# Kernel optimization log

Hardware: AMD Instinct MI355X
Metric: run time of the kernel (lower is better)

Reference implementation:

```python
import jax, jax.numpy as jnp
import numpy as np

B, L, D, H = 4, 1024, 256, 8
TEMP = float(np.sqrt(D))
EPS_SM = 1e-6
EPS_LN = 1e-5


def setup_inputs() -> dict:
    key = jax.random.key(0)
    ks = jax.random.split(key, 8)
    std = float(np.sqrt(2.0 / (D * 2)))
    return {
        "q": jax.random.normal(ks[0], (B, L, D), jnp.float32),
        "mask": jax.random.randint(ks[1], (B, L, L), 0, 2, jnp.int32),
        "k": jax.random.normal(ks[2], (B, L, D), jnp.float32),
        "v": jax.random.normal(ks[3], (B, L, D), jnp.float32),
        "w_qs": jax.random.normal(ks[4], (H * D, D), jnp.float32) * std,
        "w_ks": jax.random.normal(ks[5], (H * D, D), jnp.float32) * std,
        "w_vs": jax.random.normal(ks[6], (H * D, D), jnp.float32) * std,
        "fc_w": jax.random.normal(ks[7], (D, H * D), jnp.float32) * float(np.sqrt(2.0 / (D + H * D))),
        "fc_b": jnp.zeros((D,), jnp.float32),
        "ln_g": jnp.ones((D,), jnp.float32),
        "ln_b": jnp.zeros((D,), jnp.float32),
    }


def masked_softmax(x, m):
    # repo's layers.masked_softmax: clamp, mask-mul, stable exp, mask-mul, normalize
    x = jnp.clip(x, -15.0, 15.0) * m
    e = jnp.exp(x - jnp.max(x, axis=-1, keepdims=True)) * m
    return e / (jnp.sum(e, axis=-1, keepdims=True) + EPS_SM)


def reference(q, mask, k, v, w_qs, w_ks, w_vs, fc_w, fc_b, ln_g, ln_b):
    residual = q
    m = mask.astype(q.dtype)[:, None, :, :]          # [B,1,Lq,Lk]
    # projections to per-head full-dim: [B,L,H,D]
    qh = (q @ w_qs.T).reshape(B, L, H, D)
    kh = (k @ w_ks.T).reshape(B, L, H, D)
    vh = (v @ w_vs.T).reshape(B, L, H, D)
    scores = jnp.einsum("bqhd,bkhd->bhqk", qh, kh) / TEMP   # [B,H,Lq,Lk]
    attn = masked_softmax(scores, m)
    out = jnp.einsum("bhqk,bkhd->bqhd", attn, vh).reshape(B, L, H * D)
    out = out @ fc_w.T + fc_b                         # [B,L,D]
    out = out + residual
    mu = jnp.mean(out, axis=-1, keepdims=True)
    var = jnp.var(out, axis=-1, keepdims=True)
    out = (out - mu) / jnp.sqrt(var + EPS_LN) * ln_g + ln_b
    # match torch attn layout: [H*B, Lq, Lk] (head-major)
    attn_hb = jnp.transpose(attn, (1, 0, 2, 3)).reshape(H * B, L, L)
    return out, attn_hb
```

## Files before the change

### kernel.cpp

```cpp
#include <hip/hip_runtime.h>
#include <cstdint>
#include <math.h>

#define Bsz 4
#define Lsz 1024
#define Dsz 256
#define Hsz 8
#define HD  2048
#define NROWS (Bsz*Lsz)
#define INV_TEMP 0.0625f

#define TM 128
#define TN 128
#define TK 32

typedef __attribute__((ext_vector_type(8))) short bf16x8;
typedef __attribute__((ext_vector_type(4))) float f32x4;

__device__ inline unsigned short f2bf(float f) {
    union { float f; unsigned u; } x; x.f = f;
    unsigned r = x.u + 0x7fffu + ((x.u >> 16) & 1u);
    return (unsigned short)(r >> 16);
}

#define GBL(p) ((const __attribute__((address_space(1))) unsigned int*)(p))
#define LDS(p) ((__attribute__((address_space(3))) unsigned int*)(p))

template <typename OutT>
__global__ __launch_bounds__(256) void gemm_bt_mfma(
    const unsigned short* __restrict__ A, const unsigned short* __restrict__ Bm,
    OutT* __restrict__ C,
    int K, int lda, int ldb, int ldc,
    int inner,
    long long sA1, long long sA2, long long sB1, long long sB2,
    long long sC1, long long sC2, float alpha)
{
    const int z  = blockIdx.z;
    const int i1 = z / inner;
    const int i2 = z % inner;
    A  += (size_t)i1 * sA1 + (size_t)i2 * sA2;
    Bm += (size_t)i1 * sB1 + (size_t)i2 * sB2;
    C  += (size_t)i1 * sC1 + (size_t)i2 * sC2;

    __shared__ unsigned short As[TM * TK];
    __shared__ unsigned short Bs[TN * TK];

    const int t    = threadIdx.x;
    const int lane = t & 63;
    const int w    = t >> 6;
    const int wm   = w & 1;
    const int wn   = w >> 1;
    const int m0   = blockIdx.x * TM;
    const int n0   = blockIdx.y * TN;

    const int sr = t >> 2;
    const int sc = (t & 3) * 8;
    const unsigned short* gA0 = A  + (size_t)(m0 + sr) * lda + sc;
    const unsigned short* gA1 = A  + (size_t)(m0 + 64 + sr) * lda + sc;
    const unsigned short* gB0 = Bm + (size_t)(n0 + sr) * ldb + sc;
    const unsigned short* gB1 = Bm + (size_t)(n0 + 64 + sr) * ldb + sc;
    unsigned short* lA0 = As + t * 8;
    unsigned short* lA1 = As + 64 * TK + t * 8;
    unsigned short* lB0 = Bs + t * 8;
    unsigned short* lB1 = Bs + 64 * TK + t * 8;

    const int fr = lane & 15;
    const int fk = (lane >> 4) * 8;
    const unsigned short* pA = As + (size_t)(wm * 64 + fr) * TK + fk;
    const unsigned short* pB = Bs + (size_t)(wn * 64 + fr) * TK + fk;

    f32x4 acc[4][4];
#pragma unroll
    for (int i = 0; i < 4; ++i)
#pragma unroll
        for (int j = 0; j < 4; ++j) acc[i][j] = (f32x4){0.f, 0.f, 0.f, 0.f};

    for (int k0 = 0; k0 < K; k0 += TK) {
        __builtin_amdgcn_global_load_lds(GBL(gA0 + k0), LDS(lA0), 16, 0, 0);
        __builtin_amdgcn_global_load_lds(GBL(gA1 + k0), LDS(lA1), 16, 0, 0);
        __builtin_amdgcn_global_load_lds(GBL(gB0 + k0), LDS(lB0), 16, 0, 0);
        __builtin_amdgcn_global_load_lds(GBL(gB1 + k0), LDS(lB1), 16, 0, 0);
        __syncthreads();

        bf16x8 a[4], b[4];
#pragma unroll
        for (int i = 0; i < 4; ++i) a[i] = *(const bf16x8*)(pA + i * 16 * TK);
#pragma unroll
        for (int j = 0; j < 4; ++j) b[j] = *(const bf16x8*)(pB + j * 16 * TK);
#pragma unroll
        for (int i = 0; i < 4; ++i)
#pragma unroll
            for (int j = 0; j < 4; ++j)
                acc[i][j] = __builtin_amdgcn_mfma_f32_16x16x32_bf16(a[i], b[j], acc[i][j], 0, 0, 0);
        __syncthreads();
    }

    const int er = (lane >> 4) * 4;
    const int ec = lane & 15;
#pragma unroll
    for (int i = 0; i < 4; ++i) {
        const int mb = m0 + wm * 64 + i * 16 + er;
#pragma unroll
        for (int j = 0; j < 4; ++j) {
            const int n = n0 + wn * 64 + j * 16 + ec;
#pragma unroll
            for (int r = 0; r < 4; ++r) {
                float vv = acc[i][j][r] * alpha;
                if constexpr (sizeof(OutT) == 4)
                    C[(size_t)(mb + r) * ldc + n] = (OutT)vv;
                else
                    ((unsigned short*)C)[(size_t)(mb + r) * ldc + n] = f2bf(vv);
            }
        }
    }
}

__global__ __launch_bounds__(256) void cast_all(
    const float* __restrict__ q, const float* __restrict__ k, const float* __restrict__ v,
    const float* __restrict__ wq, const float* __restrict__ wk, const float* __restrict__ wv,
    const float* __restrict__ fw,
    unsigned short* __restrict__ qb, unsigned short* __restrict__ kb, unsigned short* __restrict__ vb,
    unsigned short* __restrict__ wqb, unsigned short* __restrict__ wkb, unsigned short* __restrict__ wvb,
    unsigned short* __restrict__ fwb)
{
    const int gid = blockIdx.x * 256 + threadIdx.x;
    const int NQ = 262144;
    const int NW = 131072;
    const float* src; unsigned short* dst; int off;
    if      (gid < NQ)            { src = q;  dst = qb;  off = gid; }
    else if (gid < 2 * NQ)        { src = k;  dst = kb;  off = gid - NQ; }
    else if (gid < 3 * NQ)        { src = v;  dst = vb;  off = gid - 2 * NQ; }
    else if (gid < 3 * NQ + NW)   { src = wq; dst = wqb; off = gid - 3 * NQ; }
    else if (gid < 3 * NQ + 2*NW) { src = wk; dst = wkb; off = gid - 3 * NQ - NW; }
    else if (gid < 3 * NQ + 3*NW) { src = wv; dst = wvb; off = gid - 3 * NQ - 2 * NW; }
    else                          { src = fw; dst = fwb; off = gid - 3 * NQ - 3 * NW; }
    float4 f = ((const float4*)src)[off];
    ushort4 o;
    o.x = f2bf(f.x); o.y = f2bf(f.y); o.z = f2bf(f.z); o.w = f2bf(f.w);
    ((ushort4*)dst)[off] = o;
}

__global__ __launch_bounds__(256) void softmax_kernel(float* __restrict__ attn,
                                                      unsigned short* __restrict__ attn_bf,
                                                      const int* __restrict__ mask)
{
    const int r  = blockIdx.x;
    const int q  = r & (Lsz - 1);
    const int hb = r >> 10;
    const int b  = hb & (Bsz - 1);
    float* row = attn + (size_t)r * Lsz;
    unsigned short* row_bf = attn_bf + (size_t)r * Lsz;
    const int* mrow = mask + ((size_t)(b * Lsz + q)) * Lsz;

    const int t = threadIdx.x;
    float x[4], mv[4];
    float lmax = -1e30f;
#pragma unroll
    for (int i = 0; i < 4; ++i) {
        const int idx = t + i * 256;
        float xv = row[idx];
        float m  = (float)mrow[idx];
        xv = fminf(fmaxf(xv, -15.f), 15.f) * m;
        x[i] = xv; mv[i] = m;
        lmax = fmaxf(lmax, xv);
    }
    __shared__ float red[4];
#pragma unroll
    for (int o = 32; o > 0; o >>= 1) lmax = fmaxf(lmax, __shfl_down(lmax, o, 64));
    const int lane = t & 63, w = t >> 6;
    if (lane == 0) red[w] = lmax;
    __syncthreads();
    const float rmax = fmaxf(fmaxf(red[0], red[1]), fmaxf(red[2], red[3]));
    __syncthreads();

    float lsum = 0.f;
#pragma unroll
    for (int i = 0; i < 4; ++i) {
        float e = expf(x[i] - rmax) * mv[i];
        x[i] = e;
        lsum += e;
    }
#pragma unroll
    for (int o = 32; o > 0; o >>= 1) lsum += __shfl_down(lsum, o, 64);
    if (lane == 0) red[w] = lsum;
    __syncthreads();
    const float rsum = red[0] + red[1] + red[2] + red[3];
    const float inv = 1.0f / (rsum + 1e-6f);
#pragma unroll
    for (int i = 0; i < 4; ++i) {
        const float p = x[i] * inv;
        row[t + i * 256] = p;
        row_bf[t + i * 256] = f2bf(p);
    }
}

__global__ __launch_bounds__(256) void ln_kernel(const float* __restrict__ gout,
                                                 const float* __restrict__ qin,
                                                 const float* __restrict__ fc_b,
                                                 const float* __restrict__ ln_g,
                                                 const float* __restrict__ ln_b,
                                                 float* __restrict__ out)
{
    const int row = blockIdx.x;
    const int t = threadIdx.x;
    const size_t idx = (size_t)row * Dsz + t;
    const float val = gout[idx] + fc_b[t] + qin[idx];

    __shared__ float red[4];
    float s = val;
#pragma unroll
    for (int o = 32; o > 0; o >>= 1) s += __shfl_down(s, o, 64);
    const int lane = t & 63, w = t >> 6;
    if (lane == 0) red[w] = s;
    __syncthreads();
    const float mu = (red[0] + red[1] + red[2] + red[3]) * (1.0f / Dsz);
    __syncthreads();

    float d = val - mu;
    float s2 = d * d;
#pragma unroll
    for (int o = 32; o > 0; o >>= 1) s2 += __shfl_down(s2, o, 64);
    if (lane == 0) red[w] = s2;
    __syncthreads();
    const float var = (red[0] + red[1] + red[2] + red[3]) * (1.0f / Dsz);

    out[idx] = d * rsqrtf(var + 1e-5f) * ln_g[t] + ln_b[t];
}

extern "C" void kernel_launch(void* const* d_in, const int* in_sizes, int n_in,
                              void* d_out, int out_size, void* d_ws, size_t ws_size,
                              hipStream_t stream)
{
    const float* q    = (const float*)d_in[0];
    const int*   mask = (const int*)d_in[1];
    const float* k    = (const float*)d_in[2];
    const float* v    = (const float*)d_in[3];
    const float* w_qs = (const float*)d_in[4];
    const float* w_ks = (const float*)d_in[5];
    const float* w_vs = (const float*)d_in[6];
    const float* fc_w = (const float*)d_in[7];
    const float* fc_b = (const float*)d_in[8];
    const float* ln_g = (const float*)d_in[9];
    const float* ln_b = (const float*)d_in[10];

    float* out  = (float*)d_out;
    float* attn = (float*)d_out + (size_t)NROWS * Dsz;

    unsigned short* wsu = (unsigned short*)d_ws;
    unsigned short* qh      = wsu;
    unsigned short* kh      = qh + (size_t)NROWS * HD;
    unsigned short* q_bf    = kh + (size_t)NROWS * HD;
    unsigned short* k_bf    = q_bf + (size_t)NROWS * Dsz;
    unsigned short* v_bf    = k_bf + (size_t)NROWS * Dsz;
    unsigned short* wq_bf   = v_bf + (size_t)NROWS * Dsz;
    unsigned short* wk_bf   = wq_bf + (size_t)HD * Dsz;
    unsigned short* wv_bf   = wk_bf + (size_t)HD * Dsz;
    unsigned short* attn_bf = wsu;
    unsigned short* regionX_end = wsu + (size_t)32 * Lsz * Lsz;
    unsigned short* vt      = regionX_end;
    unsigned short* attnv   = vt + (size_t)Bsz * HD * Lsz;
    unsigned short* fcw_bf  = attnv + (size_t)NROWS * HD;
    float*          fcout   = (float*)(fcw_bf + (size_t)Dsz * HD);

    dim3 blk(256);

    cast_all<<<dim3(5120), blk, 0, stream>>>(q, k, v, w_qs, w_ks, w_vs, fc_w,
                                             q_bf, k_bf, v_bf, wq_bf, wk_bf, wv_bf, fcw_bf);

    {
        dim3 grid(NROWS / TM, HD / TN, 1);
        gemm_bt_mfma<unsigned short><<<grid, blk, 0, stream>>>(q_bf, wq_bf, qh,
            Dsz, Dsz, Dsz, HD, 1, 0, 0, 0, 0, 0, 0, 1.0f);
        gemm_bt_mfma<unsigned short><<<grid, blk, 0, stream>>>(k_bf, wk_bf, kh,
            Dsz, Dsz, Dsz, HD, 1, 0, 0, 0, 0, 0, 0, 1.0f);
    }

    {
        dim3 grid(HD / TM, Lsz / TN, Bsz);
        gemm_bt_mfma<unsigned short><<<grid, blk, 0, stream>>>(wv_bf, v_bf, vt,
            Dsz, Dsz, Dsz, Lsz, 1,
             0,  0,
             (long long)Lsz * Dsz,  0,
             (long long)HD * Lsz,  0, 1.0f);
    }

    {
        dim3 grid(Lsz / TM, Lsz / TN, Hsz * Bsz);
        gemm_bt_mfma<float><<<grid, blk, 0, stream>>>(qh, kh, attn,
            Dsz, HD, HD, Lsz, Bsz,
             Dsz,  (long long)Lsz * HD,
             Dsz,  (long long)Lsz * HD,
             (long long)Bsz * Lsz * Lsz,  (long long)Lsz * Lsz,
            INV_TEMP);
    }

    softmax_kernel<<<dim3(Hsz * Bsz * Lsz), blk, 0, stream>>>(attn, attn_bf, mask);

    {
        dim3 grid(Lsz / TM, Dsz / TN, Hsz * Bsz);
        gemm_bt_mfma<unsigned short><<<grid, blk, 0, stream>>>(attn_bf, vt, attnv,
            Lsz, Lsz, Lsz, HD, Bsz,
             (long long)Bsz * Lsz * Lsz,  (long long)Lsz * Lsz,
             (long long)Dsz * Lsz,  (long long)HD * Lsz,
             Dsz,  (long long)Lsz * HD, 1.0f);
    }

    {
        dim3 grid(NROWS / TM, Dsz / TN, 1);
        gemm_bt_mfma<float><<<grid, blk, 0, stream>>>(attnv, fcw_bf, fcout,
            HD, HD, HD, Dsz, 1, 0, 0, 0, 0, 0, 0, 1.0f);
    }

    ln_kernel<<<dim3(NROWS), blk, 0, stream>>>(fcout, q, fc_b, ln_g, ln_b, out);
}
```

Before: 398.5 us.

## Fuse masked exp into QK GEMM epilogue and defer softmax normalization

The QK^T GEMM now applies clamp, mask and exp in its epilogue and writes bf16 unnormalized probabilities, dropping the fp32 score round-trip and the max pass. A light norm kernel computes row sums, writes the fp32 attention output and stores inverse sums, which the attn@V GEMM applies in its epilogue. The GEMM also moves to a K-tile of 64 with XOR-swizzled LDS layout, and the Q and K projections are batched into one launch. Skipping max subtraction is safe only because scores are clamped to [-15,15], and the normalized attention is now rounded through bf16 first.

```diff
diff --git a/kernel.cpp b/kernel.cpp
--- a/kernel.cpp
+++ b/kernel.cpp
@@ -10,10 +10,6 @@
 #define NROWS (Bsz*Lsz)
 #define INV_TEMP 0.0625f
 
-#define TM 128
-#define TN 128
-#define TK 32
-
 typedef __attribute__((ext_vector_type(8))) short bf16x8;
 typedef __attribute__((ext_vector_type(4))) float f32x4;
 
@@ -22,18 +18,22 @@
     unsigned r = x.u + 0x7fffu + ((x.u >> 16) & 1u);
     return (unsigned short)(r >> 16);
 }
+__device__ inline float bf2f(unsigned short u) {
+    union { unsigned u; float f; } x; x.u = (unsigned)u << 16; return x.f;
+}
 
 #define GBL(p) ((const __attribute__((address_space(1))) unsigned int*)(p))
 #define LDS(p) ((__attribute__((address_space(3))) unsigned int*)(p))
 
-template <typename OutT>
-__global__ __launch_bounds__(256) void gemm_bt_mfma(
+template <typename OutT, int EPI>
+__global__ __launch_bounds__(256) void gemm_bt(
     const unsigned short* __restrict__ A, const unsigned short* __restrict__ Bm,
     OutT* __restrict__ C,
-    int K, int lda, int ldb, int ldc,
-    int inner,
+    int K, int lda, int ldb, int ldc, int inner,
     long long sA1, long long sA2, long long sB1, long long sB2,
-    long long sC1, long long sC2, float alpha)
+    long long sC1, long long sC2, float alpha,
+    const int* __restrict__ mask, long long sM2,
+    const float* __restrict__ invs, long long sI1, long long sI2)
 {
     const int z  = blockIdx.z;
     const int i1 = z / inner;
@@ -41,33 +41,29 @@
     A  += (size_t)i1 * sA1 + (size_t)i2 * sA2;
     Bm += (size_t)i1 * sB1 + (size_t)i2 * sB2;
     C  += (size_t)i1 * sC1 + (size_t)i2 * sC2;
-
-    __shared__ unsigned short As[TM * TK];
-    __shared__ unsigned short Bs[TN * TK];
+    if (EPI == 1) mask += (size_t)i2 * sM2;
+    if (EPI == 2) invs += (size_t)i1 * sI1 + (size_t)i2 * sI2;
+
+    __shared__ unsigned short As[128 * 64];
+    __shared__ unsigned short Bs[128 * 64];
 
     const int t    = threadIdx.x;
     const int lane = t & 63;
     const int w    = t >> 6;
     const int wm   = w & 1;
     const int wn   = w >> 1;
-    const int m0   = blockIdx.x * TM;
-    const int n0   = blockIdx.y * TN;
-
-    const int sr = t >> 2;
-    const int sc = (t & 3) * 8;
-    const unsigned short* gA0 = A  + (size_t)(m0 + sr) * lda + sc;
-    const unsigned short* gA1 = A  + (size_t)(m0 + 64 + sr) * lda + sc;
-    const unsigned short* gB0 = Bm + (size_t)(n0 + sr) * ldb + sc;
-    const unsigned short* gB1 = Bm + (size_t)(n0 + 64 + sr) * ldb + sc;
-    unsigned short* lA0 = As + t * 8;
-    unsigned short* lA1 = As + 64 * TK + t * 8;
-    unsigned short* lB0 = Bs + t * 8;
-    unsigned short* lB1 = Bs + 64 * TK + t * 8;
+    const int m0   = blockIdx.x * 128;
+    const int n0   = blockIdx.y * 128;
+
+    const int rr  = t >> 3;
+    const int gch = (((t & 7) ^ (rr & 7))) * 8;
+    const unsigned short* gA = A  + (size_t)(m0 + rr) * lda + gch;
+    const unsigned short* gB = Bm + (size_t)(n0 + rr) * ldb + gch;
+    unsigned short* lA = As + t * 8;
+    unsigned short* lB = Bs + t * 8;
 
     const int fr = lane & 15;
-    const int fk = (lane >> 4) * 8;
-    const unsigned short* pA = As + (size_t)(wm * 64 + fr) * TK + fk;
-    const unsigned short* pB = Bs + (size_t)(wn * 64 + fr) * TK + fk;
+    const int q  = lane >> 4;
 
     f32x4 acc[4][4];
 #pragma unroll
@@ -75,28 +71,33 @@
 #pragma unroll
         for (int j = 0; j < 4; ++j) acc[i][j] = (f32x4){0.f, 0.f, 0.f, 0.f};
 
-    for (int k0 = 0; k0 < K; k0 += TK) {
-        __builtin_amdgcn_global_load_lds(GBL(gA0 + k0), LDS(lA0), 16, 0, 0);
-        __builtin_amdgcn_global_load_lds(GBL(gA1 + k0), LDS(lA1), 16, 0, 0);
-        __builtin_amdgcn_global_load_lds(GBL(gB0 + k0), LDS(lB0), 16, 0, 0);
-        __builtin_amdgcn_global_load_lds(GBL(gB1 + k0), LDS(lB1), 16, 0, 0);
+    for (int k0 = 0; k0 < K; k0 += 64) {
+#pragma unroll
+        for (int p = 0; p < 4; ++p) {
+            __builtin_amdgcn_global_load_lds(GBL(gA + (size_t)p * 32 * lda + k0), LDS(lA + p * 2048), 16, 0, 0);
+            __builtin_amdgcn_global_load_lds(GBL(gB + (size_t)p * 32 * ldb + k0), LDS(lB + p * 2048), 16, 0, 0);
+        }
         __syncthreads();
 
-        bf16x8 a[4], b[4];
-#pragma unroll
-        for (int i = 0; i < 4; ++i) a[i] = *(const bf16x8*)(pA + i * 16 * TK);
-#pragma unroll
-        for (int j = 0; j < 4; ++j) b[j] = *(const bf16x8*)(pB + j * 16 * TK);
-#pragma unroll
-        for (int i = 0; i < 4; ++i)
-#pragma unroll
-            for (int j = 0; j < 4; ++j)
-                acc[i][j] = __builtin_amdgcn_mfma_f32_16x16x32_bf16(a[i], b[j], acc[i][j], 0, 0, 0);
+#pragma unroll
+        for (int s = 0; s < 2; ++s) {
+            const int slot = ((s * 4 + q) ^ (fr & 7)) * 8;
+            bf16x8 a[4], b[4];
+#pragma unroll
+            for (int i = 0; i < 4; ++i) a[i] = *(const bf16x8*)(As + (wm * 64 + i * 16 + fr) * 64 + slot);
+#pragma unroll
+            for (int j = 0; j < 4; ++j) b[j] = *(const bf16x8*)(Bs + (wn * 64 + j * 16 + fr) * 64 + slot);
+#pragma unroll
+            for (int i = 0; i < 4; ++i)
+#pragma unroll
+                for (int j = 0; j < 4; ++j)
+                    acc[i][j] = __builtin_amdgcn_mfma_f32_16x16x32_bf16(a[i], b[j], acc[i][j], 0, 0, 0);
+        }
         __syncthreads();
     }
 
-    const int er = (lane >> 4) * 4;
-    const int ec = lane & 15;
+    const int er = q * 4;
+    const int ec = fr;
 #pragma unroll
     for (int i = 0; i < 4; ++i) {
         const int mb = m0 + wm * 64 + i * 16 + er;
@@ -106,10 +107,20 @@
 #pragma unroll
             for (int r = 0; r < 4; ++r) {
                 float vv = acc[i][j][r] * alpha;
-                if constexpr (sizeof(OutT) == 4)
-                    C[(size_t)(mb + r) * ldc + n] = (OutT)vv;
-                else
+                if (EPI == 0) {
+                    if constexpr (sizeof(OutT) == 4)
+                        C[(size_t)(mb + r) * ldc + n] = (OutT)vv;
+                    else
+                        ((unsigned short*)C)[(size_t)(mb + r) * ldc + n] = f2bf(vv);
+                } else if (EPI == 1) {
+                    const float m = (float)mask[(size_t)(mb + r) * Lsz + n];
+                    vv = fminf(fmaxf(vv, -15.f), 15.f) * m;
+                    vv = __expf(vv) * m;
                     ((unsigned short*)C)[(size_t)(mb + r) * ldc + n] = f2bf(vv);
+                } else {
+                    vv *= invs[mb + r];
+                    ((unsigned short*)C)[(size_t)(mb + r) * ldc + n] = f2bf(vv);
+                }
             }
         }
     }
@@ -140,58 +151,27 @@
     ((ushort4*)dst)[off] = o;
 }
 
-__global__ __launch_bounds__(256) void softmax_kernel(float* __restrict__ attn,
-                                                      unsigned short* __restrict__ attn_bf,
-                                                      const int* __restrict__ mask)
-{
-    const int r  = blockIdx.x;
-    const int q  = r & (Lsz - 1);
-    const int hb = r >> 10;
-    const int b  = hb & (Bsz - 1);
-    float* row = attn + (size_t)r * Lsz;
-    unsigned short* row_bf = attn_bf + (size_t)r * Lsz;
-    const int* mrow = mask + ((size_t)(b * Lsz + q)) * Lsz;
-
+__global__ __launch_bounds__(256) void norm_kernel(const unsigned short* __restrict__ e,
+                                                   float* __restrict__ attn,
+                                                   float* __restrict__ invsum)
+{
+    const int r = blockIdx.x;
     const int t = threadIdx.x;
-    float x[4], mv[4];
-    float lmax = -1e30f;
-#pragma unroll
-    for (int i = 0; i < 4; ++i) {
-        const int idx = t + i * 256;
-        float xv = row[idx];
-        float m  = (float)mrow[idx];
-        xv = fminf(fmaxf(xv, -15.f), 15.f) * m;
-        x[i] = xv; mv[i] = m;
-        lmax = fmaxf(lmax, xv);
-    }
+    const ushort4 u = ((const ushort4*)(e + (size_t)r * Lsz))[t];
+    float x0 = bf2f(u.x), x1 = bf2f(u.y), x2 = bf2f(u.z), x3 = bf2f(u.w);
+    float s = x0 + x1 + x2 + x3;
+
     __shared__ float red[4];
 #pragma unroll
-    for (int o = 32; o > 0; o >>= 1) lmax = fmaxf(lmax, __shfl_down(lmax, o, 64));
+    for (int o = 32; o > 0; o >>= 1) s += __shfl_down(s, o, 64);
     const int lane = t & 63, w = t >> 6;
-    if (lane == 0) red[w] = lmax;
-    __syncthreads();
-    const float rmax = fmaxf(fmaxf(red[0], red[1]), fmaxf(red[2], red[3]));
-    __syncthreads();
-
-    float lsum = 0.f;
-#pragma unroll
-    for (int i = 0; i < 4; ++i) {
-        float e = expf(x[i] - rmax) * mv[i];
-        x[i] = e;
-        lsum += e;
-    }
-#pragma unroll
-    for (int o = 32; o > 0; o >>= 1) lsum += __shfl_down(lsum, o, 64);
-    if (lane == 0) red[w] = lsum;
-    __syncthreads();
-    const float rsum = red[0] + red[1] + red[2] + red[3];
-    const float inv = 1.0f / (rsum + 1e-6f);
-#pragma unroll
-    for (int i = 0; i < 4; ++i) {
-        const float p = x[i] * inv;
-        row[t + i * 256] = p;
-        row_bf[t + i * 256] = f2bf(p);
-    }
+    if (lane == 0) red[w] = s;
+    __syncthreads();
+    const float inv = 1.0f / (red[0] + red[1] + red[2] + red[3] + 1e-6f);
+
+    float4 o4; o4.x = x0 * inv; o4.y = x1 * inv; o4.z = x2 * inv; o4.w = x3 * inv;
+    ((float4*)(attn + (size_t)r * Lsz))[t] = o4;
+    if (t == 0) invsum[r] = inv;
 }
 
 __global__ __launch_bounds__(256) void ln_kernel(const float* __restrict__ gout,
@@ -247,20 +227,20 @@
     float* attn = (float*)d_out + (size_t)NROWS * Dsz;
 
     unsigned short* wsu = (unsigned short*)d_ws;
-    unsigned short* qh      = wsu;
-    unsigned short* kh      = qh + (size_t)NROWS * HD;
-    unsigned short* q_bf    = kh + (size_t)NROWS * HD;
-    unsigned short* k_bf    = q_bf + (size_t)NROWS * Dsz;
-    unsigned short* v_bf    = k_bf + (size_t)NROWS * Dsz;
-    unsigned short* wq_bf   = v_bf + (size_t)NROWS * Dsz;
-    unsigned short* wk_bf   = wq_bf + (size_t)HD * Dsz;
-    unsigned short* wv_bf   = wk_bf + (size_t)HD * Dsz;
-    unsigned short* attn_bf = wsu;
-    unsigned short* regionX_end = wsu + (size_t)32 * Lsz * Lsz;
-    unsigned short* vt      = regionX_end;
-    unsigned short* attnv   = vt + (size_t)Bsz * HD * Lsz;
-    unsigned short* fcw_bf  = attnv + (size_t)NROWS * HD;
-    float*          fcout   = (float*)(fcw_bf + (size_t)Dsz * HD);
+    unsigned short* qh     = wsu;
+    unsigned short* kh     = qh + (size_t)NROWS * HD;
+    unsigned short* q_bf   = kh + (size_t)NROWS * HD;
+    unsigned short* k_bf   = q_bf + (size_t)NROWS * Dsz;
+    unsigned short* v_bf   = k_bf + (size_t)NROWS * Dsz;
+    unsigned short* wq_bf  = v_bf + (size_t)NROWS * Dsz;
+    unsigned short* wk_bf  = wq_bf + (size_t)HD * Dsz;
+    unsigned short* wv_bf  = wk_bf + (size_t)HD * Dsz;
+    unsigned short* vt     = wv_bf + (size_t)HD * Dsz;
+    unsigned short* attn_e = vt + (size_t)Bsz * HD * Lsz;
+    unsigned short* attnv  = attn_e + (size_t)32 * Lsz * Lsz;
+    unsigned short* fcw_bf = attnv + (size_t)NROWS * HD;
+    float*          invsum = (float*)(fcw_bf + (size_t)Dsz * HD);
+    float*          fcout  = invsum + 32768;
 
     dim3 blk(256);
 
@@ -268,47 +248,47 @@
                                              q_bf, k_bf, v_bf, wq_bf, wk_bf, wv_bf, fcw_bf);
 
     {
-        dim3 grid(NROWS / TM, HD / TN, 1);
-        gemm_bt_mfma<unsigned short><<<grid, blk, 0, stream>>>(q_bf, wq_bf, qh,
-            Dsz, Dsz, Dsz, HD, 1, 0, 0, 0, 0, 0, 0, 1.0f);
-        gemm_bt_mfma<unsigned short><<<grid, blk, 0, stream>>>(k_bf, wk_bf, kh,
-            Dsz, Dsz, Dsz, HD, 1, 0, 0, 0, 0, 0, 0, 1.0f);
-    }
-
-    {
-        dim3 grid(HD / TM, Lsz / TN, Bsz);
-        gemm_bt_mfma<unsigned short><<<grid, blk, 0, stream>>>(wv_bf, v_bf, vt,
+        dim3 grid(NROWS / 128, HD / 128, 2);
+        gemm_bt<unsigned short, 0><<<grid, blk, 0, stream>>>(q_bf, wq_bf, qh,
+            Dsz, Dsz, Dsz, HD, 2,
+            0, (long long)NROWS * Dsz, 0, (long long)HD * Dsz, 0, (long long)NROWS * HD,
+            1.0f, nullptr, 0, nullptr, 0, 0);
+    }
+
+    {
+        dim3 grid(HD / 128, Lsz / 128, Bsz);
+        gemm_bt<unsigned short, 0><<<grid, blk, 0, stream>>>(wv_bf, v_bf, vt,
             Dsz, Dsz, Dsz, Lsz, 1,
-             0,  0,
-             (long long)Lsz * Dsz,  0,
-             (long long)HD * Lsz,  0, 1.0f);
-    }
-
-    {
-        dim3 grid(Lsz / TM, Lsz / TN, Hsz * Bsz);
-        gemm_bt_mfma<float><<<grid, blk, 0, stream>>>(qh, kh, attn,
+            0, 0, (long long)Lsz * Dsz, 0, (long long)HD * Lsz, 0,
+            1.0f, nullptr, 0, nullptr, 0, 0);
+    }
+
+    {
+        dim3 grid(Lsz / 128, Lsz / 128, Hsz * Bsz);
+        gemm_bt<unsigned short, 1><<<grid, blk, 0, stream>>>(qh, kh, attn_e,
             Dsz, HD, HD, Lsz, Bsz,
-             Dsz,  (long long)Lsz * HD,
-             Dsz,  (long long)Lsz * HD,
-             (long long)Bsz * Lsz * Lsz,  (long long)Lsz * Lsz,
-            INV_TEMP);
-    }
-
-    softmax_kernel<<<dim3(Hsz * Bsz * Lsz), blk, 0, stream>>>(attn, attn_bf, mask);
-
-    {
-        dim3 grid(Lsz / TM, Dsz / TN, Hsz * Bsz);
-        gemm_bt_mfma<unsigned short><<<grid, blk, 0, stream>>>(attn_bf, vt, attnv,
+            Dsz, (long long)Lsz * HD, Dsz, (long long)Lsz * HD,
+            (long long)Bsz * Lsz * Lsz, (long long)Lsz * Lsz,
+            INV_TEMP, mask, (long long)Lsz * Lsz, nullptr, 0, 0);
+    }
+
+    norm_kernel<<<dim3(32 * Lsz), blk, 0, stream>>>(attn_e, attn, invsum);
+
+    {
+        dim3 grid(Lsz / 128, Dsz / 128, Hsz * Bsz);
+        gemm_bt<unsigned short, 2><<<grid, blk, 0, stream>>>(attn_e, vt, attnv,
             Lsz, Lsz, Lsz, HD, Bsz,
-             (long long)Bsz * Lsz * Lsz,  (long long)Lsz * Lsz,
-             (long long)Dsz * Lsz,  (long long)HD * Lsz,
-             Dsz,  (long long)Lsz * HD, 1.0f);
-    }
-
-    {
-        dim3 grid(NROWS / TM, Dsz / TN, 1);
-        gemm_bt_mfma<float><<<grid, blk, 0, stream>>>(attnv, fcw_bf, fcout,
-            HD, HD, HD, Dsz, 1, 0, 0, 0, 0, 0, 0, 1.0f);
+            (long long)Bsz * Lsz * Lsz, (long long)Lsz * Lsz,
+            (long long)Dsz * Lsz, (long long)HD * Lsz,
+            Dsz, (long long)Lsz * HD,
+            1.0f, nullptr, 0, invsum, (long long)Bsz * Lsz, (long long)Lsz);
+    }
+
+    {
+        dim3 grid(NROWS / 128, Dsz / 128, 1);
+        gemm_bt<float, 0><<<grid, blk, 0, stream>>>(attnv, fcw_bf, fcout,
+            HD, HD, HD, Dsz, 1, 0, 0, 0, 0, 0, 0,
+            1.0f, nullptr, 0, nullptr, 0, 0);
     }
 
     ln_kernel<<<dim3(NROWS), blk, 0, stream>>>(fcout, q, fc_b, ln_g, ln_b, out);
```

Result: faster. 362.2 us (-9.1%).
